# Performance work log

Hardware: AMD Instinct MI355X
Metric: run time of the kernel (lower is better)

## Reference

```python
import jax, jax.numpy as jnp
import numpy as np

DIM, HID = 1024, 2048
N_SHARED, N_ROUTED, TOP_K = 2, 6, 2
AUX_W = 0.01
B, T = 4, 2048


def _swiglu(x, w1, w2, w3):
    # x: [N, C]; w1,w3: [C, H]; w2: [H, C]
    return (jax.nn.silu(x @ w1) * (x @ w3)) @ w2


def setup_inputs() -> dict:
    key = jax.random.key(0)
    ks = jax.random.split(key, 9)
    s = 0.02
    return {
        "x": jax.random.normal(ks[0], (B, T, DIM), dtype=jnp.float32),
        "w1_s": jax.random.normal(ks[1], (N_SHARED, DIM, HID), dtype=jnp.float32) * s,
        "w2_s": jax.random.normal(ks[2], (N_SHARED, HID, DIM), dtype=jnp.float32) * s,
        "w3_s": jax.random.normal(ks[3], (N_SHARED, DIM, HID), dtype=jnp.float32) * s,
        "w1_r": jax.random.normal(ks[4], (N_ROUTED, DIM, HID), dtype=jnp.float32) * s,
        "w2_r": jax.random.normal(ks[5], (N_ROUTED, HID, DIM), dtype=jnp.float32) * s,
        "w3_r": jax.random.normal(ks[6], (N_ROUTED, DIM, HID), dtype=jnp.float32) * s,
        "gate_w": jax.random.normal(ks[7], (DIM, N_ROUTED), dtype=jnp.float32) * s,
        "out_w": jax.random.normal(ks[8], (DIM, DIM), dtype=jnp.float32) * s,
    }


def reference(x, w1_s, w2_s, w3_s, w1_r, w2_r, w3_r, gate_w, out_w):
    Bv, Tv, C = x.shape
    xf = x.reshape(-1, C)  # [N, C]

    # shared experts: always run for every token
    shared = jnp.zeros_like(xf)
    for e in range(N_SHARED):
        shared = shared + _swiglu(xf, w1_s[e], w2_s[e], w3_s[e])

    # router
    logits = xf @ gate_w                       # [N, E]
    wk, idx = jax.lax.top_k(logits, TOP_K)     # [N, K]
    wk = jax.nn.softmax(wk, axis=-1)           # softmax over selected k only

    # routed experts: dense per-expert pass scaled by (zero for unselected) weight
    routed = jnp.zeros_like(xf)
    for e in range(N_ROUTED):
        we = jnp.sum(wk * (idx == e).astype(xf.dtype), axis=-1, keepdims=True)  # [N,1]
        routed = routed + we * _swiglu(xf, w1_r[e], w2_r[e], w3_r[e])

    combined = shared + routed

    # aux load-balance loss (top-1 assignment fraction x mean prob)
    probs = jax.nn.softmax(logits, axis=-1)
    f_i = jnp.mean(jax.nn.one_hot(idx[:, 0], N_ROUTED, dtype=xf.dtype), axis=0)
    p_i = jnp.mean(probs, axis=0)
    aux_loss = AUX_W * N_ROUTED * jnp.sum(f_i * p_i)

    out = (combined @ out_w).reshape(Bv, Tv, C)
    return out, aux_loss
```

## Files before the change

### kernel.cpp

```cpp
#include <hip/hip_runtime.h>
#include <hip/hip_bf16.h>
#include <cstdint>

#define DIMc 1024
#define HIDc 2048
#define NTOK 8192
#define NRT 6

typedef __bf16 bf16x8 __attribute__((ext_vector_type(8)));
typedef __bf16 bf16x4 __attribute__((ext_vector_type(4)));
typedef float  f32x4  __attribute__((ext_vector_type(4)));

__device__ __forceinline__ void gl_lds16(const void* gsrc, void* ldst) {
    auto g = (const __attribute__((address_space(1))) void*)gsrc;
    auto l = (__attribute__((address_space(3))) void*)ldst;
    __builtin_amdgcn_global_load_lds(g, l, 16, 0, 0);
}

__global__ __launch_bounds__(256) void tcvt_k(
    const float* __restrict__ w1s, const float* __restrict__ w2s, const float* __restrict__ w3s,
    const float* __restrict__ w1r, const float* __restrict__ w2r, const float* __restrict__ w3r,
    const float* __restrict__ outw,
    __bf16* __restrict__ W13T, __bf16* __restrict__ W2T, __bf16* __restrict__ OutWT)
{
    int id = blockIdx.z;
    const float* src; __bf16* dst; int K, N;
    if (id < 16) {
        int ex = id >> 1, half = id & 1;
        const float* w1 = (ex < 2) ? w1s + (size_t)ex * DIMc * HIDc : w1r + (size_t)(ex - 2) * DIMc * HIDc;
        const float* w3 = (ex < 2) ? w3s + (size_t)ex * DIMc * HIDc : w3r + (size_t)(ex - 2) * DIMc * HIDc;
        src = half ? w3 : w1;
        K = 1024; N = 2048;
        dst = W13T + (size_t)ex * 4096 * 1024 + (size_t)half * 2048 * 1024;
    } else if (id < 24) {
        int ex = id - 16;
        src = (ex < 2) ? w2s + (size_t)ex * HIDc * DIMc : w2r + (size_t)(ex - 2) * HIDc * DIMc;
        K = 2048; N = 1024;
        dst = W2T + (size_t)ex * 2048 * 1024;
    } else {
        src = outw; K = 1024; N = 1024; dst = OutWT;
    }
    int n0 = blockIdx.x * 32, k0 = blockIdx.y * 32;
    if (n0 >= N || k0 >= K) return;
    __shared__ float t[32][33];
    int c = threadIdx.x & 31, rb = threadIdx.x >> 5;
#pragma unroll
    for (int i = 0; i < 4; i++) {
        int r = rb + i * 8;
        t[r][c] = src[(size_t)(k0 + r) * N + n0 + c];
    }
    __syncthreads();
#pragma unroll
    for (int i = 0; i < 4; i++) {
        int r = rb + i * 8;
        dst[(size_t)(n0 + r) * K + k0 + c] = (__bf16)t[c][r];
    }
}

__global__ __launch_bounds__(256) void router_k(
    const float* __restrict__ x, const float* __restrict__ gate,
    __bf16* __restrict__ xb, int* __restrict__ tke, float* __restrict__ tkw,
    float* __restrict__ auxp, float* __restrict__ auxf, int* __restrict__ rcnt)
{
    __shared__ float gl[DIMc * NRT];
    __shared__ float pacc[NRT];
    __shared__ int hist1[NRT], hist2[NRT];
    for (int i = threadIdx.x; i < DIMc * NRT; i += 256) gl[i] = gate[i];
    if (threadIdx.x < NRT) { pacc[threadIdx.x] = 0.f; hist1[threadIdx.x] = 0; hist2[threadIdx.x] = 0; }
    __syncthreads();
    int lane = threadIdx.x & 63, wid = threadIdx.x >> 6;
    for (int rep = 0; rep < 4; rep++) {
        int t = blockIdx.x * 16 + wid * 4 + rep;
        float a[NRT] = {0.f, 0.f, 0.f, 0.f, 0.f, 0.f};
        const float* xr = x + (size_t)t * DIMc;
        __bf16* xbr = xb + (size_t)t * DIMc;
        for (int k = lane; k < DIMc; k += 64) {
            float v = xr[k];
            xbr[k] = (__bf16)v;
#pragma unroll
            for (int e = 0; e < NRT; e++) a[e] += v * gl[k * NRT + e];
        }
#pragma unroll
        for (int e = 0; e < NRT; e++)
#pragma unroll
            for (int m = 32; m; m >>= 1) a[e] += __shfl_xor(a[e], m);
        if (lane == 0) {
            int i0 = 0; float m0 = a[0];
#pragma unroll
            for (int e = 1; e < NRT; e++) if (a[e] > m0) { m0 = a[e]; i0 = e; }
            int i1 = -1; float m1 = -1e30f;
#pragma unroll
            for (int e = 0; e < NRT; e++) if (e != i0 && a[e] > m1) { m1 = a[e]; i1 = e; }
            float w1 = __expf(m1 - m0);
            float inv = 1.f / (1.f + w1);
            tke[2 * t] = i0; tke[2 * t + 1] = i1;
            tkw[2 * t] = inv; tkw[2 * t + 1] = w1 * inv;
            float se = 0.f, pe[NRT];
#pragma unroll
            for (int e = 0; e < NRT; e++) { pe[e] = __expf(a[e] - m0); se += pe[e]; }
            float rinv = 1.f / se;
#pragma unroll
            for (int e = 0; e < NRT; e++) atomicAdd(&pacc[e], pe[e] * rinv);
            atomicAdd(&hist1[i0], 1);
            atomicAdd(&hist2[i0], 1); atomicAdd(&hist2[i1], 1);
        }
    }
    __syncthreads();
    if (threadIdx.x < NRT) {
        atomicAdd(&auxp[threadIdx.x], pacc[threadIdx.x]);
        atomicAdd(&auxf[threadIdx.x], (float)hist1[threadIdx.x]);
        atomicAdd(&rcnt[threadIdx.x], hist2[threadIdx.x]);
    }
}

__global__ void offsets_k(const int* __restrict__ rcnt, int* __restrict__ goff, int* __restrict__ gcnt) {
    if (threadIdx.x == 0) {
        goff[0] = 0; goff[1] = NTOK; gcnt[0] = NTOK; gcnt[1] = NTOK;
        int off = 0;
        for (int e = 0; e < NRT; e++) { goff[2 + e] = off; gcnt[2 + e] = rcnt[e]; off += rcnt[e]; }
    }
}

__global__ __launch_bounds__(256) void scatter_k(
    const int* __restrict__ tke, const float* __restrict__ tkw,
    const int* __restrict__ goff, int* __restrict__ curs,
    int* __restrict__ perm, float* __restrict__ wrow)
{
    int t = blockIdx.x * 256 + threadIdx.x;
    if (t >= NTOK) return;
    perm[t] = t;        wrow[t] = 1.f;
    perm[NTOK + t] = t; wrow[NTOK + t] = 1.f;
#pragma unroll
    for (int k = 0; k < 2; k++) {
        int e = tke[2 * t + k]; float w = tkw[2 * t + k];
        int slot = atomicAdd(&curs[e], 1);
        int pos = 2 * NTOK + goff[2 + e] + slot;
        perm[pos] = t; wrow[pos] = w;
    }
}

__global__ void auxfin_k(const float* __restrict__ auxp, const float* __restrict__ auxf, float* __restrict__ out) {
    if (threadIdx.x == 0) {
        float s = 0.f;
        for (int e = 0; e < NRT; e++) s += (auxf[e] * (1.f / NTOK)) * (auxp[e] * (1.f / NTOK));
        out[(size_t)NTOK * DIMc] = 0.01f * 6.f * s;
    }
}

template <int MODE>
__global__ __launch_bounds__(256, 2) void gemm_k(
    const __bf16* __restrict__ A, const __bf16* __restrict__ Bbase,
    float* __restrict__ outF, __bf16* __restrict__ outB,
    const int* __restrict__ goff, const int* __restrict__ gcnt,
    const int* __restrict__ perm, const float* __restrict__ wrow,
    int gbase, int pbase, int K)
{
    constexpr int NT = (MODE == 0) ? 3 : 2;
    __shared__ __bf16 lds[NT * 128 * 64];
    __bf16* As  = lds;
    __bf16* B1s = lds + 128 * 64;
    __bf16* B3s = (MODE == 0) ? lds + 2 * 128 * 64 : lds;

    const int g = gbase + blockIdx.z;
    const int cnt = gcnt[g];
    const int bx = blockIdx.x, by = blockIdx.y;
    if (bx * 128 >= cnt) return;
    const int gofs = goff[g];
    const int tid = threadIdx.x;
    const int lane = tid & 63, wid = tid >> 6;
    const int wr = wid >> 1, wc = wid & 1;
    const int l15 = lane & 15, l4 = lane >> 4;

    const __bf16* Bg;
    if constexpr (MODE == 0)      Bg = Bbase + (size_t)g * (4096 * 1024);
    else if constexpr (MODE == 1) Bg = Bbase + (size_t)g * (2048 * 1024);
    else                          Bg = Bbase;

    const __bf16* agA[4]; const __bf16* agB1[4]; const __bf16* agB3[4];
    int ldsOfs[4];
#pragma unroll
    for (int i = 0; i < 4; i++) {
        int chunk = i * 256 + tid;
        int row = chunk >> 3, c8 = chunk & 7;
        int cg = c8 ^ (row & 7);
        int r = bx * 128 + row; if (r > cnt - 1) r = cnt - 1;
        size_t arow;
        if constexpr (MODE == 0)      arow = (size_t)perm[pbase + gofs + r];
        else if constexpr (MODE == 1) arow = (size_t)(gofs + r);
        else                          arow = (size_t)r;
        agA[i] = A + arow * (size_t)K + cg * 8;
        int nr = by * 128 + row;
        agB1[i] = Bg + (size_t)nr * K + cg * 8;
        if constexpr (MODE == 0) agB3[i] = Bg + (size_t)(2048 + nr) * K + cg * 8;
        ldsOfs[i] = chunk * 8;
    }

    f32x4 acc1[4][4], acc3[4][4];
#pragma unroll
    for (int mi = 0; mi < 4; mi++)
#pragma unroll
        for (int ni = 0; ni < 4; ni++)
#pragma unroll
            for (int j = 0; j < 4; j++) { acc1[mi][ni][j] = 0.f; acc3[mi][ni][j] = 0.f; }

    const int nkt = K >> 6;
    for (int kt = 0; kt < nkt; kt++) {
        __syncthreads();
#pragma unroll
        for (int i = 0; i < 4; i++) {
            gl_lds16(agA[i] + kt * 64, &As[ldsOfs[i]]);
            gl_lds16(agB1[i] + kt * 64, &B1s[ldsOfs[i]]);
            if constexpr (MODE == 0) gl_lds16(agB3[i] + kt * 64, &B3s[ldsOfs[i]]);
        }
        asm volatile("s_waitcnt vmcnt(0)" ::: "memory");
        __syncthreads();
#pragma unroll
        for (int kk = 0; kk < 64; kk += 32) {
            bf16x8 av[4];
#pragma unroll
            for (int mi = 0; mi < 4; mi++) {
                int lr = wr * 64 + mi * 16 + l15;
                int cr = ((kk >> 3) + l4) ^ (lr & 7);
                av[mi] = *(const bf16x8*)&As[lr * 64 + cr * 8];
            }
#pragma unroll
            for (int ni = 0; ni < 4; ni++) {
                int lr = wc * 64 + ni * 16 + l15;
                int cr = ((kk >> 3) + l4) ^ (lr & 7);
                bf16x8 bv = *(const bf16x8*)&B1s[lr * 64 + cr * 8];
                if constexpr (MODE == 0) {
                    bf16x8 bv3 = *(const bf16x8*)&B3s[lr * 64 + cr * 8];
#pragma unroll
                    for (int mi = 0; mi < 4; mi++) {
                        acc1[mi][ni] = __builtin_amdgcn_mfma_f32_16x16x32_bf16(av[mi], bv,  acc1[mi][ni], 0, 0, 0);
                        acc3[mi][ni] = __builtin_amdgcn_mfma_f32_16x16x32_bf16(av[mi], bv3, acc3[mi][ni], 0, 0, 0);
                    }
                } else {
#pragma unroll
                    for (int mi = 0; mi < 4; mi++)
                        acc1[mi][ni] = __builtin_amdgcn_mfma_f32_16x16x32_bf16(av[mi], bv, acc1[mi][ni], 0, 0, 0);
                }
            }
        }
    }

#pragma unroll
    for (int mi = 0; mi < 4; mi++) {
#pragma unroll
        for (int j = 0; j < 4; j++) {
            int r = bx * 128 + wr * 64 + mi * 16 + l4 * 4 + j;
            if (r < cnt) {
                if constexpr (MODE == 0) {
                    size_t orow = (size_t)(gofs + r) * 2048;
#pragma unroll
                    for (int ni = 0; ni < 4; ni++) {
                        int c = by * 128 + wc * 64 + ni * 16 + l15;
                        float h1 = acc1[mi][ni][j], h3 = acc3[mi][ni][j];
                        float sg = h1 / (1.f + __expf(-h1));
                        outB[orow + c] = (__bf16)(sg * h3);
                    }
                } else if constexpr (MODE == 1) {
                    int pos = pbase + gofs + r;
                    int tok = perm[pos]; float w = wrow[pos];
                    size_t orow = (size_t)tok * 1024;
#pragma unroll
                    for (int ni = 0; ni < 4; ni++) {
                        int c = by * 128 + wc * 64 + ni * 16 + l15;
                        atomicAdd(&outF[orow + c], w * acc1[mi][ni][j]);
                    }
                } else {
                    size_t orow = (size_t)r * 1024;
#pragma unroll
                    for (int ni = 0; ni < 4; ni++) {
                        int c = by * 128 + wc * 64 + ni * 16 + l15;
                        outF[orow + c] = acc1[mi][ni][j];
                    }
                }
            }
        }
    }
}

__global__ __launch_bounds__(256) void cvtcomb_k(const float* __restrict__ c, __bf16* __restrict__ cb) {
    size_t i = (size_t)blockIdx.x * 256 + threadIdx.x;
    const float4* s = (const float4*)c;
    float4 v = s[i];
    bf16x4 o; o[0] = (__bf16)v.x; o[1] = (__bf16)v.y; o[2] = (__bf16)v.z; o[3] = (__bf16)v.w;
    ((bf16x4*)cb)[i] = o;
}

extern "C" void kernel_launch(void* const* d_in, const int* in_sizes, int n_in,
                              void* d_out, int out_size, void* d_ws, size_t ws_size,
                              hipStream_t stream) {
    const float* x    = (const float*)d_in[0];
    const float* w1s  = (const float*)d_in[1];
    const float* w2s  = (const float*)d_in[2];
    const float* w3s  = (const float*)d_in[3];
    const float* w1r  = (const float*)d_in[4];
    const float* w2r  = (const float*)d_in[5];
    const float* w3r  = (const float*)d_in[6];
    const float* gate = (const float*)d_in[7];
    const float* outw = (const float*)d_in[8];
    float* out = (float*)d_out;

    char* ws = (char*)d_ws;
    float* combined = (float*)ws;
    float* auxp = (float*)(ws + 33554432);
    float* auxf = auxp + 8;
    int*   rcnt = (int*)(ws + 33554432 + 64);
    int*   curs = rcnt + 8;
    size_t off = 33554432 + 256;
    __bf16* xb    = (__bf16*)(ws + off); off += 16777216;
    __bf16* W13T  = (__bf16*)(ws + off); off += 67108864;
    __bf16* W2T   = (__bf16*)(ws + off); off += 33554432;
    __bf16* OutWT = (__bf16*)(ws + off); off += 2097152;
    __bf16* gbuf  = (__bf16*)(ws + off); off += 67108864;
    __bf16* cb    = gbuf;
    int*   tke  = (int*)(ws + off);   off += 65536;
    float* tkw  = (float*)(ws + off); off += 65536;
    int*   perm = (int*)(ws + off);   off += 131072;
    float* wrow = (float*)(ws + off); off += 131072;
    int*   goffp = (int*)(ws + off);  off += 64;
    int*   gcntp = (int*)(ws + off);  off += 64;

    hipMemsetAsync(d_ws, 0, 33554432 + 256, stream);

    dim3 b256(256);
    tcvt_k<<<dim3(64, 64, 25), b256, 0, stream>>>(w1s, w2s, w3s, w1r, w2r, w3r, outw, W13T, W2T, OutWT);
    router_k<<<dim3(512), b256, 0, stream>>>(x, gate, xb, tke, tkw, auxp, auxf, rcnt);
    offsets_k<<<dim3(1), dim3(64), 0, stream>>>(rcnt, goffp, gcntp);
    scatter_k<<<dim3(32), b256, 0, stream>>>(tke, tkw, goffp, curs, perm, wrow);
    auxfin_k<<<dim3(1), dim3(64), 0, stream>>>(auxp, auxf, out);

    gemm_k<0><<<dim3(64, 16, 2), b256, 0, stream>>>(xb, W13T, nullptr, gbuf, goffp, gcntp, perm, wrow, 0, 0, 1024);
    gemm_k<1><<<dim3(64, 8, 2),  b256, 0, stream>>>(gbuf, W2T, combined, nullptr, goffp, gcntp, perm, wrow, 0, 0, 2048);
    gemm_k<0><<<dim3(64, 16, 6), b256, 0, stream>>>(xb, W13T, nullptr, gbuf, goffp, gcntp, perm, wrow, 2, 16384, 1024);
    gemm_k<1><<<dim3(64, 8, 6),  b256, 0, stream>>>(gbuf, W2T, combined, nullptr, goffp, gcntp, perm, wrow, 2, 16384, 2048);

    cvtcomb_k<<<dim3(8192), b256, 0, stream>>>(combined, cb);
    gemm_k<2><<<dim3(64, 8, 1), b256, 0, stream>>>(cb, OutWT, out, nullptr, goffp, gcntp, perm, wrow, 0, 0, 1024);
}
```

Baseline: 980.7 us.

## Double-buffer GEMM LDS loads, split gate/up GEMM, add XCD swizzle

```diff
diff --git a/kernel.cpp b/kernel.cpp
--- a/kernel.cpp
+++ b/kernel.cpp
@@ -9,12 +9,23 @@
 
 typedef __bf16 bf16x8 __attribute__((ext_vector_type(8)));
 typedef __bf16 bf16x4 __attribute__((ext_vector_type(4)));
+typedef __bf16 bf16x2v __attribute__((ext_vector_type(2)));
 typedef float  f32x4  __attribute__((ext_vector_type(4)));
+
+#define VMCNT(n) asm volatile("s_waitcnt vmcnt(" #n ")" ::: "memory")
+#define RBAR()   asm volatile("s_barrier" ::: "memory")
 
 __device__ __forceinline__ void gl_lds16(const void* gsrc, void* ldst) {
     auto g = (const __attribute__((address_space(1))) void*)gsrc;
     auto l = (__attribute__((address_space(3))) void*)ldst;
     __builtin_amdgcn_global_load_lds(g, l, 16, 0, 0);
+}
+
+__device__ __forceinline__ void xcd_swz(int lid, int nwg, int gx, int& bx, int& by) {
+    int q = nwg >> 3, r = nwg & 7;
+    int xcd = lid & 7, idx = lid >> 3;
+    int nlid = (xcd < r ? xcd * (q + 1) : r * (q + 1) + (xcd - r) * q) + idx;
+    bx = nlid % gx; by = nlid / gx;
 }
 
 __global__ __launch_bounds__(256) void tcvt_k(
@@ -50,10 +61,12 @@
         t[r][c] = src[(size_t)(k0 + r) * N + n0 + c];
     }
     __syncthreads();
-#pragma unroll
-    for (int i = 0; i < 4; i++) {
-        int r = rb + i * 8;
-        dst[(size_t)(n0 + r) * K + k0 + c] = (__bf16)t[c][r];
+    int kp = threadIdx.x & 15, nn = threadIdx.x >> 4;
+#pragma unroll
+    for (int pass = 0; pass < 2; pass++) {
+        int n = nn + pass * 16;
+        bf16x2v v; v[0] = (__bf16)t[2 * kp][n]; v[1] = (__bf16)t[2 * kp + 1][n];
+        *(bf16x2v*)&dst[(size_t)(n0 + n) * K + k0 + 2 * kp] = v;
     }
 }
 
@@ -147,23 +160,127 @@
     }
 }
 
+__global__ __launch_bounds__(512, 2) void gemm13_k(
+    const __bf16* __restrict__ A, const __bf16* __restrict__ Bbase, __bf16* __restrict__ outB,
+    const int* __restrict__ goff, const int* __restrict__ gcnt, const int* __restrict__ perm,
+    int gbase, int pbase)
+{
+    __shared__ __bf16 lds[2 * 32768];
+    const int g = gbase + blockIdx.z;
+    const int cnt = gcnt[g];
+    int bx, by;
+    xcd_swz(blockIdx.x + gridDim.x * blockIdx.y, gridDim.x * gridDim.y, gridDim.x, bx, by);
+    if (bx * 256 >= cnt) return;
+    const int gofs = goff[g];
+    const int tid = threadIdx.x;
+    const int lane = tid & 63, wid = tid >> 6;
+    const int wr = wid >> 1, wc = wid & 1;
+    const int l15 = lane & 15, l4 = lane >> 4;
+
+    const __bf16* Bg = Bbase + (size_t)g * (4096 * 1024);
+
+    const __bf16* agA[4]; const __bf16* agB1[2]; const __bf16* agB3[2];
+    int ldsA[4], ldsB[2];
+#pragma unroll
+    for (int i = 0; i < 4; i++) {
+        int chunk = i * 512 + tid;
+        int row = chunk >> 3, cg = (chunk & 7) ^ (row & 7);
+        int r = bx * 256 + row; if (r > cnt - 1) r = cnt - 1;
+        agA[i] = A + (size_t)perm[pbase + gofs + r] * 1024 + cg * 8;
+        ldsA[i] = chunk * 8;
+    }
+#pragma unroll
+    for (int i = 0; i < 2; i++) {
+        int chunk = i * 512 + tid;
+        int row = chunk >> 3, cg = (chunk & 7) ^ (row & 7);
+        int nr = by * 128 + row;
+        agB1[i] = Bg + (size_t)nr * 1024 + cg * 8;
+        agB3[i] = Bg + (size_t)(2048 + nr) * 1024 + cg * 8;
+        ldsB[i] = chunk * 8;
+    }
+
+#define STAGE13(b, kt) { __bf16* d_ = lds + (b) * 32768; \
+    _Pragma("unroll") for (int i_ = 0; i_ < 4; i_++) gl_lds16(agA[i_] + (kt) * 64, d_ + ldsA[i_]); \
+    _Pragma("unroll") for (int i_ = 0; i_ < 2; i_++) { \
+        gl_lds16(agB1[i_] + (kt) * 64, d_ + 16384 + ldsB[i_]); \
+        gl_lds16(agB3[i_] + (kt) * 64, d_ + 24576 + ldsB[i_]); } }
+
+    f32x4 acc1[4][4], acc3[4][4];
+#pragma unroll
+    for (int mi = 0; mi < 4; mi++)
+#pragma unroll
+        for (int ni = 0; ni < 4; ni++)
+#pragma unroll
+            for (int j = 0; j < 4; j++) { acc1[mi][ni][j] = 0.f; acc3[mi][ni][j] = 0.f; }
+
+    const int nkt = 16;
+    STAGE13(0, 0);
+    for (int kt = 0; kt < nkt; kt++) {
+        const int cur = kt & 1;
+        if (kt + 1 < nkt) { STAGE13(cur ^ 1, kt + 1); VMCNT(8); }
+        else              { VMCNT(0); }
+        RBAR();
+        const __bf16* As  = lds + cur * 32768;
+        const __bf16* B1s = As + 16384;
+        const __bf16* B3s = As + 24576;
+#pragma unroll
+        for (int kk = 0; kk < 64; kk += 32) {
+            bf16x8 av[4];
+#pragma unroll
+            for (int mi = 0; mi < 4; mi++) {
+                int lr = wr * 64 + mi * 16 + l15;
+                int cr = ((kk >> 3) + l4) ^ (lr & 7);
+                av[mi] = *(const bf16x8*)&As[lr * 64 + cr * 8];
+            }
+#pragma unroll
+            for (int ni = 0; ni < 4; ni++) {
+                int lr = wc * 64 + ni * 16 + l15;
+                int cr = ((kk >> 3) + l4) ^ (lr & 7);
+                bf16x8 bv1 = *(const bf16x8*)&B1s[lr * 64 + cr * 8];
+                bf16x8 bv3 = *(const bf16x8*)&B3s[lr * 64 + cr * 8];
+#pragma unroll
+                for (int mi = 0; mi < 4; mi++) {
+                    acc1[mi][ni] = __builtin_amdgcn_mfma_f32_16x16x32_bf16(av[mi], bv1, acc1[mi][ni], 0, 0, 0);
+                    acc3[mi][ni] = __builtin_amdgcn_mfma_f32_16x16x32_bf16(av[mi], bv3, acc3[mi][ni], 0, 0, 0);
+                }
+            }
+        }
+        RBAR();
+    }
+
+#pragma unroll
+    for (int mi = 0; mi < 4; mi++) {
+#pragma unroll
+        for (int j = 0; j < 4; j++) {
+            int r = bx * 256 + wr * 64 + mi * 16 + l4 * 4 + j;
+            if (r < cnt) {
+                size_t orow = (size_t)(gofs + r) * 2048;
+#pragma unroll
+                for (int ni = 0; ni < 4; ni++) {
+                    int c = by * 128 + wc * 64 + ni * 16 + l15;
+                    float h1 = acc1[mi][ni][j], h3 = acc3[mi][ni][j];
+                    float sg = h1 / (1.f + __expf(-h1));
+                    outB[orow + c] = (__bf16)(sg * h3);
+                }
+            }
+        }
+    }
+#undef STAGE13
+}
+
 template <int MODE>
-__global__ __launch_bounds__(256, 2) void gemm_k(
+__global__ __launch_bounds__(256, 2) void gemmNN_k(
     const __bf16* __restrict__ A, const __bf16* __restrict__ Bbase,
-    float* __restrict__ outF, __bf16* __restrict__ outB,
+    float* __restrict__ outF,
     const int* __restrict__ goff, const int* __restrict__ gcnt,
     const int* __restrict__ perm, const float* __restrict__ wrow,
     int gbase, int pbase, int K)
 {
-    constexpr int NT = (MODE == 0) ? 3 : 2;
-    __shared__ __bf16 lds[NT * 128 * 64];
-    __bf16* As  = lds;
-    __bf16* B1s = lds + 128 * 64;
-    __bf16* B3s = (MODE == 0) ? lds + 2 * 128 * 64 : lds;
-
+    __shared__ __bf16 lds[2 * 16384];
     const int g = gbase + blockIdx.z;
     const int cnt = gcnt[g];
-    const int bx = blockIdx.x, by = blockIdx.y;
+    int bx, by;
+    xcd_swz(blockIdx.x + gridDim.x * blockIdx.y, gridDim.x * gridDim.y, gridDim.x, bx, by);
     if (bx * 128 >= cnt) return;
     const int gofs = goff[g];
     const int tid = threadIdx.x;
@@ -171,49 +288,43 @@
     const int wr = wid >> 1, wc = wid & 1;
     const int l15 = lane & 15, l4 = lane >> 4;
 
-    const __bf16* Bg;
-    if constexpr (MODE == 0)      Bg = Bbase + (size_t)g * (4096 * 1024);
-    else if constexpr (MODE == 1) Bg = Bbase + (size_t)g * (2048 * 1024);
-    else                          Bg = Bbase;
-
-    const __bf16* agA[4]; const __bf16* agB1[4]; const __bf16* agB3[4];
-    int ldsOfs[4];
+    const __bf16* Bg = (MODE == 1) ? Bbase + (size_t)g * (2048 * 1024) : Bbase;
+
+    const __bf16* agA[4]; const __bf16* agB[4];
+    int ldsOf[4];
 #pragma unroll
     for (int i = 0; i < 4; i++) {
         int chunk = i * 256 + tid;
-        int row = chunk >> 3, c8 = chunk & 7;
-        int cg = c8 ^ (row & 7);
+        int row = chunk >> 3, cg = (chunk & 7) ^ (row & 7);
         int r = bx * 128 + row; if (r > cnt - 1) r = cnt - 1;
-        size_t arow;
-        if constexpr (MODE == 0)      arow = (size_t)perm[pbase + gofs + r];
-        else if constexpr (MODE == 1) arow = (size_t)(gofs + r);
-        else                          arow = (size_t)r;
+        size_t arow = (MODE == 1) ? (size_t)(gofs + r) : (size_t)r;
         agA[i] = A + arow * (size_t)K + cg * 8;
-        int nr = by * 128 + row;
-        agB1[i] = Bg + (size_t)nr * K + cg * 8;
-        if constexpr (MODE == 0) agB3[i] = Bg + (size_t)(2048 + nr) * K + cg * 8;
-        ldsOfs[i] = chunk * 8;
-    }
-
-    f32x4 acc1[4][4], acc3[4][4];
+        agB[i] = Bg + (size_t)(by * 128 + row) * K + cg * 8;
+        ldsOf[i] = chunk * 8;
+    }
+
+#define STAGENN(b, kt) { __bf16* d_ = lds + (b) * 16384; \
+    _Pragma("unroll") for (int i_ = 0; i_ < 4; i_++) { \
+        gl_lds16(agA[i_] + (kt) * 64, d_ + ldsOf[i_]); \
+        gl_lds16(agB[i_] + (kt) * 64, d_ + 8192 + ldsOf[i_]); } }
+
+    f32x4 acc[4][4];
 #pragma unroll
     for (int mi = 0; mi < 4; mi++)
 #pragma unroll
         for (int ni = 0; ni < 4; ni++)
 #pragma unroll
-            for (int j = 0; j < 4; j++) { acc1[mi][ni][j] = 0.f; acc3[mi][ni][j] = 0.f; }
+            for (int j = 0; j < 4; j++) acc[mi][ni][j] = 0.f;
 
     const int nkt = K >> 6;
+    STAGENN(0, 0);
     for (int kt = 0; kt < nkt; kt++) {
-        __syncthreads();
-#pragma unroll
-        for (int i = 0; i < 4; i++) {
-            gl_lds16(agA[i] + kt * 64, &As[ldsOfs[i]]);
-            gl_lds16(agB1[i] + kt * 64, &B1s[ldsOfs[i]]);
-            if constexpr (MODE == 0) gl_lds16(agB3[i] + kt * 64, &B3s[ldsOfs[i]]);
-        }
-        asm volatile("s_waitcnt vmcnt(0)" ::: "memory");
-        __syncthreads();
+        const int cur = kt & 1;
+        if (kt + 1 < nkt) { STAGENN(cur ^ 1, kt + 1); VMCNT(8); }
+        else              { VMCNT(0); }
+        RBAR();
+        const __bf16* As = lds + cur * 16384;
+        const __bf16* Bs = As + 8192;
 #pragma unroll
         for (int kk = 0; kk < 64; kk += 32) {
             bf16x8 av[4];
@@ -227,21 +338,13 @@
             for (int ni = 0; ni < 4; ni++) {
                 int lr = wc * 64 + ni * 16 + l15;
                 int cr = ((kk >> 3) + l4) ^ (lr & 7);
-                bf16x8 bv = *(const bf16x8*)&B1s[lr * 64 + cr * 8];
-                if constexpr (MODE == 0) {
-                    bf16x8 bv3 = *(const bf16x8*)&B3s[lr * 64 + cr * 8];
-#pragma unroll
-                    for (int mi = 0; mi < 4; mi++) {
-                        acc1[mi][ni] = __builtin_amdgcn_mfma_f32_16x16x32_bf16(av[mi], bv,  acc1[mi][ni], 0, 0, 0);
-                        acc3[mi][ni] = __builtin_amdgcn_mfma_f32_16x16x32_bf16(av[mi], bv3, acc3[mi][ni], 0, 0, 0);
-                    }
-                } else {
-#pragma unroll
-                    for (int mi = 0; mi < 4; mi++)
-                        acc1[mi][ni] = __builtin_amdgcn_mfma_f32_16x16x32_bf16(av[mi], bv, acc1[mi][ni], 0, 0, 0);
-                }
-            }
-        }
+                bf16x8 bv = *(const bf16x8*)&Bs[lr * 64 + cr * 8];
+#pragma unroll
+                for (int mi = 0; mi < 4; mi++)
+                    acc[mi][ni] = __builtin_amdgcn_mfma_f32_16x16x32_bf16(av[mi], bv, acc[mi][ni], 0, 0, 0);
+            }
+        }
+        RBAR();
     }
 
 #pragma unroll
@@ -250,35 +353,27 @@
         for (int j = 0; j < 4; j++) {
             int r = bx * 128 + wr * 64 + mi * 16 + l4 * 4 + j;
             if (r < cnt) {
-                if constexpr (MODE == 0) {
-                    size_t orow = (size_t)(gofs + r) * 2048;
-#pragma unroll
-                    for (int ni = 0; ni < 4; ni++) {
-                        int c = by * 128 + wc * 64 + ni * 16 + l15;
-                        float h1 = acc1[mi][ni][j], h3 = acc3[mi][ni][j];
-                        float sg = h1 / (1.f + __expf(-h1));
-                        outB[orow + c] = (__bf16)(sg * h3);
-                    }
-                } else if constexpr (MODE == 1) {
+                if constexpr (MODE == 1) {
                     int pos = pbase + gofs + r;
                     int tok = perm[pos]; float w = wrow[pos];
                     size_t orow = (size_t)tok * 1024;
 #pragma unroll
                     for (int ni = 0; ni < 4; ni++) {
                         int c = by * 128 + wc * 64 + ni * 16 + l15;
-                        atomicAdd(&outF[orow + c], w * acc1[mi][ni][j]);
+                        atomicAdd(&outF[orow + c], w * acc[mi][ni][j]);
                     }
                 } else {
                     size_t orow = (size_t)r * 1024;
 #pragma unroll
                     for (int ni = 0; ni < 4; ni++) {
                         int c = by * 128 + wc * 64 + ni * 16 + l15;
-                        outF[orow + c] = acc1[mi][ni][j];
+                        outF[orow + c] = acc[mi][ni][j];
                     }
                 }
             }
         }
     }
+#undef STAGENN
 }
 
 __global__ __launch_bounds__(256) void cvtcomb_k(const float* __restrict__ c, __bf16* __restrict__ cb) {
@@ -325,18 +420,18 @@
 
     hipMemsetAsync(d_ws, 0, 33554432 + 256, stream);
 
-    dim3 b256(256);
+    dim3 b256(256), b512(512);
     tcvt_k<<<dim3(64, 64, 25), b256, 0, stream>>>(w1s, w2s, w3s, w1r, w2r, w3r, outw, W13T, W2T, OutWT);
     router_k<<<dim3(512), b256, 0, stream>>>(x, gate, xb, tke, tkw, auxp, auxf, rcnt);
     offsets_k<<<dim3(1), dim3(64), 0, stream>>>(rcnt, goffp, gcntp);
     scatter_k<<<dim3(32), b256, 0, stream>>>(tke, tkw, goffp, curs, perm, wrow);
     auxfin_k<<<dim3(1), dim3(64), 0, stream>>>(auxp, auxf, out);
 
-    gemm_k<0><<<dim3(64, 16, 2), b256, 0, stream>>>(xb, W13T, nullptr, gbuf, goffp, gcntp, perm, wrow, 0, 0, 1024);
-    gemm_k<1><<<dim3(64, 8, 2),  b256, 0, stream>>>(gbuf, W2T, combined, nullptr, goffp, gcntp, perm, wrow, 0, 0, 2048);
-    gemm_k<0><<<dim3(64, 16, 6), b256, 0, stream>>>(xb, W13T, nullptr, gbuf, goffp, gcntp, perm, wrow, 2, 16384, 1024);
-    gemm_k<1><<<dim3(64, 8, 6),  b256, 0, stream>>>(gbuf, W2T, combined, nullptr, goffp, gcntp, perm, wrow, 2, 16384, 2048);
+    gemm13_k<<<dim3(32, 16, 2), b512, 0, stream>>>(xb, W13T, gbuf, goffp, gcntp, perm, 0, 0);
+    gemmNN_k<1><<<dim3(64, 8, 2), b256, 0, stream>>>(gbuf, W2T, combined, goffp, gcntp, perm, wrow, 0, 0, 2048);
+    gemm13_k<<<dim3(32, 16, 6), b512, 0, stream>>>(xb, W13T, gbuf, goffp, gcntp, perm, 2, 2 * NTOK);
+    gemmNN_k<1><<<dim3(64, 8, 6), b256, 0, stream>>>(gbuf, W2T, combined, goffp, gcntp, perm, wrow, 2, 2 * NTOK, 2048);
 
     cvtcomb_k<<<dim3(8192), b256, 0, stream>>>(combined, cb);
-    gemm_k<2><<<dim3(64, 8, 1), b256, 0, stream>>>(cb, OutWT, out, nullptr, goffp, gcntp, perm, wrow, 0, 0, 1024);
-}
+    gemmNN_k<2><<<dim3(64, 8, 1), b256, 0, stream>>>(cb, OutWT, out, goffp, gcntp, perm, wrow, 0, 0, 1024);
+}
```

After: 934.7 us. 4.7% less time.
